# Kernel optimization log

Hardware: AMD Instinct MI355X
Metric: run time of the kernel (lower is better)

## Reference

```python
import jax, jax.numpy as jnp
import numpy as np

L, B, Q, P, D, H, F = 3, 256, 128, 16, 256, 16, 512
DK = D // H
SCALE = DK ** -0.5  # lsa=False -> constant scale
EPS = 1e-5


def _ln(x, g, b):
    m = jnp.mean(x, axis=-1, keepdims=True)
    v = jnp.mean(jnp.square(x - m), axis=-1, keepdims=True)
    return (x - m) * jax.lax.rsqrt(v + EPS) * g + b


def setup_inputs() -> dict:
    key = jax.random.key(0)
    ks = jax.random.split(key, 12)
    w = lambda k, shape: 0.02 * jax.random.normal(k, shape, dtype=jnp.float32)
    return {
        "x": jax.random.normal(ks[0], (B, Q, P), dtype=jnp.float32),
        "attn_bias": 0.1 * jax.random.normal(ks[1], (1, Q, Q), dtype=jnp.float32),
        "W_P": w(ks[2], (P, D)), "b_P": jnp.zeros((D,), jnp.float32),
        "W_pos": w(ks[3], (Q, D)),
        "Wq": w(ks[4], (L, D, D)), "bq": jnp.zeros((L, D), jnp.float32),
        "Wk": w(ks[5], (L, D, D)), "bk": jnp.zeros((L, D), jnp.float32),
        "Wv": w(ks[6], (L, D, D)), "bv": jnp.zeros((L, D), jnp.float32),
        "Wo": w(ks[7], (L, D, D)), "bo": jnp.zeros((L, D), jnp.float32),
        "ln1_g": jnp.ones((L, D), jnp.float32), "ln1_b": jnp.zeros((L, D), jnp.float32),
        "W1": w(ks[8], (L, D, F)), "b1": jnp.zeros((L, F), jnp.float32),
        "W2": w(ks[9], (L, F, D)), "b2": jnp.zeros((L, D), jnp.float32),
        "ln2_g": jnp.ones((L, D), jnp.float32), "ln2_b": jnp.zeros((L, D), jnp.float32),
    }


def _encoder(x, attn_bias, W_P, b_P, W_pos,
             Wq, bq, Wk, bk, Wv, bv, Wo, bo, ln1_g, ln1_b,
             W1, b1, W2, b2, ln2_g, ln2_b):
    # patch embedding + positional encoding (dropout=0, eval mode)
    z = x @ W_P + b_P + W_pos                      # [B, Q, D]
    bias = attn_bias[:, None]                      # [1, 1, Q, Q]

    def layer(carry, p):
        z, prev = carry
        (wq, bq_, wk, bk_, wv, bv_, wo, bo_, g1, be1, w1, b1_, w2, b2_, g2, be2) = p
        q = (z @ wq + bq_).reshape(B, Q, H, DK).transpose(0, 2, 1, 3)  # [B,H,Q,dk]
        k = (z @ wk + bk_).reshape(B, Q, H, DK).transpose(0, 2, 1, 3)
        v = (z @ wv + bv_).reshape(B, Q, H, DK).transpose(0, 2, 1, 3)
        # residual-attention + bias-augmented scores
        scores = jnp.einsum('bhqd,bhkd->bhqk', q, k) * SCALE + prev + bias
        attn = jax.nn.softmax(scores, axis=-1)
        o = jnp.einsum('bhqk,bhkd->bhqd', attn, v)
        o = o.transpose(0, 2, 1, 3).reshape(B, Q, D) @ wo + bo_
        z = _ln(z + o, g1, be1)                     # post-norm
        ffo = jax.nn.gelu(z @ w1 + b1_, approximate=False) @ w2 + b2_
        z = _ln(z + ffo, g2, be2)
        return (z, scores), None

    prev0 = jnp.zeros((B, H, Q, Q), z.dtype)        # prev=None == add zero
    params = (Wq, bq, Wk, bk, Wv, bv, Wo, bo, ln1_g, ln1_b,
              W1, b1, W2, b2, ln2_g, ln2_b)
    (z, _), _ = jax.lax.scan(layer, (z, prev0), params)
    return z


def reference(x, attn_bias, W_P, b_P, W_pos, Wq, bq, Wk, bk, Wv, bv, Wo, bo,
              ln1_g, ln1_b, W1, b1, W2, b2, ln2_g, ln2_b):
    return _encoder(x, attn_bias, W_P, b_P, W_pos, Wq, bq, Wk, bk, Wv, bv,
                    Wo, bo, ln1_g, ln1_b, W1, b1, W2, b2, ln2_g, ln2_b)
```

## Files before the change

### kernel.cpp

```cpp
#include <hip/hip_runtime.h>

#define DEV __device__ __forceinline__

typedef float          f32x4  __attribute__((ext_vector_type(4)));
typedef __bf16         bf16x8 __attribute__((ext_vector_type(8)));
typedef unsigned short u16x8  __attribute__((ext_vector_type(8)));
typedef unsigned short u16x4  __attribute__((ext_vector_type(4)));

static constexpr int  Bq   = 256;
static constexpr int  Qs   = 128;
static constexpr int  Dm   = 256;
static constexpr int  Ff   = 512;
static constexpr int  ROWS = Bq * Qs;
static constexpr long QK_LSTR = (long)ROWS * 512;

DEV float b2f(unsigned short h) {
    unsigned int u = ((unsigned int)h) << 16;
    float f; __builtin_memcpy(&f, &u, 4); return f;
}
DEV unsigned short f2b(float f) {
    unsigned int u; __builtin_memcpy(&u, &f, 4);
    u += 0x7fffu + ((u >> 16) & 1u);
    return (unsigned short)(u >> 16);
}
DEV f32x4 mfma_bf16(u16x8 a, u16x8 b, f32x4 c) {
    return __builtin_amdgcn_mfma_f32_16x16x32_bf16(
        __builtin_bit_cast(bf16x8, a), __builtin_bit_cast(bf16x8, b), c, 0, 0, 0);
}
DEV void gl_lds16(const unsigned short* g, unsigned short* l) {
    __builtin_amdgcn_global_load_lds(
        (const __attribute__((address_space(1))) unsigned int*)g,
        (__attribute__((address_space(3))) unsigned int*)l, 16, 0, 0);
}

__global__ void k_embed(const float* __restrict__ x,
                        const float* __restrict__ WP,
                        const float* __restrict__ bP,
                        const float* __restrict__ Wpos,
                        unsigned short* __restrict__ zb) {
    int row = blockIdx.x;
    int d   = threadIdx.x;
    int q   = row & (Qs - 1);
    const float* xr = x + row * 16;
    float acc = bP[d] + Wpos[q * Dm + d];
#pragma unroll
    for (int p = 0; p < 16; p++) acc += xr[p] * WP[p * Dm + d];
    zb[(long)row * Dm + d] = f2b(acc);
}

static constexpr int S0 = 3 * 768 * 256;
static constexpr int S1 = 3 * 256 * 256;
static constexpr int S2 = 3 * 512 * 256;
static constexpr int S3 = 3 * 256 * 512;
static constexpr int S4 = 3 * 768;
static constexpr int S5 = 3 * 64 * 256;
static constexpr int PREP_TOT = S0 + S1 + S2 + S3 + S4 + S5;

__global__ void k_prep(const float* __restrict__ Wq, const float* __restrict__ Wk,
                       const float* __restrict__ Wv, const float* __restrict__ Wo,
                       const float* __restrict__ W1, const float* __restrict__ W2,
                       const float* __restrict__ bq, const float* __restrict__ bk,
                       const float* __restrict__ bv, const float* __restrict__ ab,
                       unsigned short* __restrict__ wTqkv, unsigned short* __restrict__ wTo,
                       unsigned short* __restrict__ wT1, unsigned short* __restrict__ wT2,
                       float* __restrict__ bqkv, float* __restrict__ pb) {
    int idx = blockIdx.x * 256 + threadIdx.x;
    if (idx < S0) {
        int l = idx / (768 * 256), r = idx % (768 * 256);
        int n = r / 256, k = r % 256;
        const float* W = (n < 256) ? Wq : (n < 512) ? Wk : Wv;
        float v = W[(long)l * 65536 + k * 256 + (n & 255)];
        if (n < 256) v *= 0.25f;
        wTqkv[idx] = f2b(v);
    } else if (idx < S0 + S1) {
        int j = idx - S0;
        int l = j / 65536, r = j % 65536, n = r / 256, k = r % 256;
        wTo[j] = f2b(Wo[(long)l * 65536 + k * 256 + n]);
    } else if (idx < S0 + S1 + S2) {
        int j = idx - S0 - S1;
        int l = j / (512 * 256), r = j % (512 * 256), n = r / 256, k = r % 256;
        wT1[j] = f2b(W1[(long)l * 131072 + k * 512 + n]);
    } else if (idx < S0 + S1 + S2 + S3) {
        int j = idx - S0 - S1 - S2;
        int l = j / (256 * 512), r = j % (256 * 512), n = r / 512, k = r % 512;
        wT2[j] = f2b(W2[(long)l * 131072 + k * 256 + n]);
    } else if (idx < S0 + S1 + S2 + S3 + S4) {
        int j = idx - S0 - S1 - S2 - S3;
        int l = j / 768, c = j % 768;
        float v = (c < 256) ? bq[l * 256 + c] * 0.25f
                : (c < 512) ? bk[l * 256 + c - 256]
                            : bv[l * 256 + c - 512];
        bqkv[j] = v;
    } else if (idx < PREP_TOT) {
        int j = idx - S0 - S1 - S2 - S3 - S4;
        int l = j / 16384, r = j % 16384;
        int u = r / 256, t = r % 256;
        int i = u >> 5, rr = (u >> 3) & 3, jj = u & 7;
        int wave = t >> 6, quad = (t >> 4) & 3, l16 = t & 15;
        int m = 32 * wave + 16 * i + 4 * quad + rr;
        int col = 16 * jj + l16;
        pb[j] = (float)(l + 1) * ab[m * 128 + col];
    }
}

template <int GELU, int MODE>
__global__ __launch_bounds__(256) void k_gemm(const unsigned short* __restrict__ A,
                                              const unsigned short* __restrict__ WT,
                                              const float* __restrict__ bias,
                                              unsigned short* __restrict__ outB,
                                              unsigned short* __restrict__ aux,
                                              int M, int N, int K) {
    __shared__ unsigned short As[2][128 * 32];
    __shared__ unsigned short Bs[2][128 * 32];
    const int tid  = threadIdx.x;
    const int wave = tid >> 6, lane = tid & 63, quad = lane >> 4, l16 = lane & 15;
    const int mq = wave >> 1, nq = wave & 1;
    const int m_blk = blockIdx.x * 128, n_blk = blockIdx.y * 128;
    const int c0 = tid, c1 = tid + 256;
    const int ra0 = c0 >> 2, ca0 = (c0 & 3) * 8;
    const int ra1 = c1 >> 2, ca1 = (c1 & 3) * 8;

    f32x4 acc[4][4] = {};

    for (int k0 = 0; k0 < K; k0 += 64) {
#pragma unroll
        for (int hh = 0; hh < 2; hh++) {
            int kk = k0 + hh * 32;
            gl_lds16(A  + (long)(m_blk + ra0) * K + kk + ca0, &As[hh][c0 * 8]);
            gl_lds16(A  + (long)(m_blk + ra1) * K + kk + ca1, &As[hh][c1 * 8]);
            gl_lds16(WT + (long)(n_blk + ra0) * K + kk + ca0, &Bs[hh][c0 * 8]);
            gl_lds16(WT + (long)(n_blk + ra1) * K + kk + ca1, &Bs[hh][c1 * 8]);
        }
        __syncthreads();
#pragma unroll
        for (int hh = 0; hh < 2; hh++) {
            u16x8 af[4], bf[4];
#pragma unroll
            for (int i = 0; i < 4; i++)
                af[i] = *(const u16x8*)&As[hh][(64 * mq + 16 * i + l16) * 32 + quad * 8];
#pragma unroll
            for (int j = 0; j < 4; j++)
                bf[j] = *(const u16x8*)&Bs[hh][(64 * nq + 16 * j + l16) * 32 + quad * 8];
#pragma unroll
            for (int i = 0; i < 4; i++)
#pragma unroll
                for (int j = 0; j < 4; j++)
                    acc[i][j] = mfma_bf16(af[i], bf[j], acc[i][j]);
        }
        __syncthreads();
    }

#pragma unroll
    for (int i = 0; i < 4; i++) {
        int row = m_blk + 64 * mq + 16 * i + quad * 4;
#pragma unroll
        for (int j = 0; j < 4; j++) {
            int col = n_blk + 64 * nq + 16 * j + l16;
            float bb = bias[col];
#pragma unroll
            for (int r = 0; r < 4; r++) {
                float v = acc[i][j][r] + bb;
                if (GELU) v = 0.5f * v * (1.0f + erff(v * 0.70710678118f));
                if (MODE == 0) outB[(long)(row + r) * N + col] = f2b(v);
                if (MODE == 2) {
                    int grow = row + r, b = grow >> 7, rin = grow & 127;
                    if (col < 512) {
                        int s = col >> 8, hh = (col >> 4) & 15, dk = col & 15;
                        outB[((long)((b * 16 + hh) * 2 + s)) * 2048 + rin * 16 + dk] = f2b(v);
                    } else {
                        aux[(long)grow * 256 + (col - 512)] = f2b(v);
                    }
                }
            }
        }
    }
}

template <int LAST>
__global__ __launch_bounds__(256) void k_gemm_ln(const unsigned short* __restrict__ A,
                                                 const unsigned short* __restrict__ WT,
                                                 const float* __restrict__ bias,
                                                 const unsigned short* __restrict__ Zres,
                                                 const float* __restrict__ g,
                                                 const float* __restrict__ be,
                                                 unsigned short* __restrict__ zb,
                                                 float* __restrict__ outF,
                                                 int K) {
    __shared__ unsigned short smem[16384 + 2048 + 8192];
    unsigned short* Zs = smem;
    unsigned short* As = smem + 16384;
    unsigned short* Bs = smem + 16384 + 2048;
    float2* stats = (float2*)(smem + 16384);

    const int tid  = threadIdx.x;
    const int wave = tid >> 6, lane = tid & 63, quad = lane >> 4, l16 = lane & 15;
    const int m_blk = blockIdx.x * 64;

#pragma unroll
    for (int s = 0; s < 8; s++) {
        int c = tid + 256 * s;
        int zr = c >> 5, zc = (c & 31) * 8;
        gl_lds16(Zres + (long)(m_blk + zr) * 256 + zc, &Zs[c * 8]);
    }

    const int ca = (tid & 3) * 8, raA = tid >> 2;
    f32x4 acc[4][4] = {};

    for (int k0 = 0; k0 < K; k0 += 32) {
        gl_lds16(A + (long)(m_blk + raA) * K + k0 + ca, &As[tid * 8]);
#pragma unroll
        for (int s = 0; s < 4; s++) {
            int c = tid + 256 * s;
            int br = c >> 2, bc = (c & 3) * 8;
            gl_lds16(WT + (long)br * K + k0 + bc, &Bs[c * 8]);
        }
        __syncthreads();
        u16x8 af[4], bf[4];
#pragma unroll
        for (int i = 0; i < 4; i++)
            af[i] = *(const u16x8*)&As[(16 * i + l16) * 32 + quad * 8];
#pragma unroll
        for (int j = 0; j < 4; j++)
            bf[j] = *(const u16x8*)&Bs[(64 * wave + 16 * j + l16) * 32 + quad * 8];
#pragma unroll
        for (int i = 0; i < 4; i++)
#pragma unroll
            for (int j = 0; j < 4; j++)
                acc[i][j] = mfma_bf16(af[i], bf[j], acc[i][j]);
        __syncthreads();
    }

    float bb[4], gg[4], bt[4];
#pragma unroll
    for (int j = 0; j < 4; j++) {
        int col = 64 * wave + 16 * j + l16;
        bb[j] = bias[col]; gg[j] = g[col]; bt[j] = be[col];
    }
#pragma unroll
    for (int i = 0; i < 4; i++) {
#pragma unroll
        for (int r = 0; r < 4; r++) {
            int rloc = 16 * i + quad * 4 + r;
            float s1 = 0.f, s2 = 0.f;
#pragma unroll
            for (int j = 0; j < 4; j++) {
                int col = 64 * wave + 16 * j + l16;
                float v = acc[i][j][r] + bb[j] + b2f(Zs[rloc * 256 + col]);
                acc[i][j][r] = v;
                s1 += v; s2 += v * v;
            }
            for (int mk = 1; mk < 16; mk <<= 1) {
                s1 += __shfl_xor(s1, mk);
                s2 += __shfl_xor(s2, mk);
            }
            if (l16 == 0) stats[rloc * 4 + wave] = make_float2(s1, s2);
        }
    }
    __syncthreads();
#pragma unroll
    for (int i = 0; i < 4; i++) {
#pragma unroll
        for (int r = 0; r < 4; r++) {
            int rloc = 16 * i + quad * 4 + r;
            f32x4 p0 = *(const f32x4*)&stats[rloc * 4];
            f32x4 p1 = *(const f32x4*)&stats[rloc * 4 + 2];
            float S1 = p0[0] + p0[2] + p1[0] + p1[2];
            float S2 = p0[1] + p0[3] + p1[1] + p1[3];
            float mean = S1 * (1.0f / 256.0f);
            float var  = S2 * (1.0f / 256.0f) - mean * mean;
            float rstd = rsqrtf(var + 1e-5f);
            long grow = m_blk + rloc;
#pragma unroll
            for (int j = 0; j < 4; j++) {
                int col = 64 * wave + 16 * j + l16;
                float o = (acc[i][j][r] - mean) * rstd * gg[j] + bt[j];
                if (LAST) outF[grow * 256 + col] = o;
                else      zb[grow * 256 + col] = f2b(o);
            }
        }
    }
}

template <int L>
__global__ __launch_bounds__(256) void k_attn(const unsigned short* __restrict__ qkh,
                                              const unsigned short* __restrict__ vbuf,
                                              const float* __restrict__ pb,
                                              unsigned short* __restrict__ o_out) {
    __shared__ unsigned short vt[16 * 136];
    __shared__ unsigned short Ps[128 * 136];
    const int tid  = threadIdx.x;
    const int wave = tid >> 6, lane = tid & 63, quad = lane >> 4, l16 = lane & 15;
    const int b = blockIdx.x >> 4, h = blockIdx.x & 15;
    const int qrow = tid >> 1, half = tid & 1;

    u16x8 vv = *(const u16x8*)(vbuf + (long)(b * Qs + qrow) * 256 + h * 16 + half * 8);
    const float* pbt = pb + (long)L * 16384 + tid;

    f32x4 accS[2][8] = {};
    u16x8 zero = {};

    constexpr int FULL = (L + 1) / 2;
    constexpr bool HALF = ((L + 1) & 1) != 0;

#pragma unroll
    for (int p = 0; p < FULL; p++) {
        const unsigned short* q0 = qkh + ((long)(((2 * p) * Bq + b) * 16 + h) * 2) * 2048;
        const unsigned short* q1 = qkh + ((long)(((2 * p + 1) * Bq + b) * 16 + h) * 2) * 2048;
        const unsigned short* qsel = (quad < 2) ? q0 : q1;
        const unsigned short* ksel = (quad < 2) ? (q0 + 2048) : (q1 + 2048);
        const int koff = (quad & 1) * 8;
        u16x8 af[2], bf8[8];
#pragma unroll
        for (int i = 0; i < 2; i++) {
            int m = 32 * wave + 16 * i + l16;
            af[i] = *(const u16x8*)(qsel + m * 16 + koff);
        }
#pragma unroll
        for (int j = 0; j < 8; j++) {
            int n = 16 * j + l16;
            bf8[j] = *(const u16x8*)(ksel + n * 16 + koff);
        }
#pragma unroll
        for (int i = 0; i < 2; i++)
#pragma unroll
            for (int j = 0; j < 8; j++)
                accS[i][j] = mfma_bf16(af[i], bf8[j], accS[i][j]);
    }
    if (HALF) {
        const unsigned short* qt = qkh + ((long)((L * Bq + b) * 16 + h) * 2) * 2048;
        const unsigned short* kt = qt + 2048;
        u16x8 af[2], bf8[8];
#pragma unroll
        for (int i = 0; i < 2; i++) {
            int m = 32 * wave + 16 * i + l16;
            af[i] = (quad < 2) ? *(const u16x8*)(qt + m * 16 + quad * 8) : zero;
        }
#pragma unroll
        for (int j = 0; j < 8; j++) {
            int n = 16 * j + l16;
            bf8[j] = (quad < 2) ? *(const u16x8*)(kt + n * 16 + quad * 8) : zero;
        }
#pragma unroll
        for (int i = 0; i < 2; i++)
#pragma unroll
            for (int j = 0; j < 8; j++)
                accS[i][j] = mfma_bf16(af[i], bf8[j], accS[i][j]);
    }

#pragma unroll
    for (int jj = 0; jj < 8; jj++) vt[(half * 8 + jj) * 136 + qrow] = vv[jj];

#pragma unroll
    for (int i = 0; i < 2; i++) {
#pragma unroll
        for (int r = 0; r < 4; r++) {
            int m = 32 * wave + 16 * i + quad * 4 + r;
#pragma unroll
            for (int j = 0; j < 8; j++) {
                int u = (i * 4 + r) * 8 + j;
                float s = accS[i][j][r] + pbt[u * 256];
                Ps[m * 136 + 16 * j + l16] = f2b(__expf(s));
            }
        }
    }
    __syncthreads();

    f32x4 accO[2] = {};
    f32x4 accR[2] = {};
    u16x8 ones;
#pragma unroll
    for (int jj = 0; jj < 8; jj++) ones[jj] = 0x3F80;
#pragma unroll
    for (int s = 0; s < 4; s++) {
        u16x8 bv = *(const u16x8*)&vt[l16 * 136 + s * 32 + quad * 8];
#pragma unroll
        for (int i = 0; i < 2; i++) {
            u16x8 ap = *(const u16x8*)&Ps[(32 * wave + 16 * i + l16) * 136 + s * 32 + quad * 8];
            accO[i] = mfma_bf16(ap, bv, accO[i]);
            accR[i] = mfma_bf16(ap, ones, accR[i]);
        }
    }
#pragma unroll
    for (int i = 0; i < 2; i++)
#pragma unroll
        for (int r = 0; r < 4; r++) {
            int m = 32 * wave + 16 * i + quad * 4 + r;
            float inv = __builtin_amdgcn_rcpf(accR[i][r]);
            o_out[(long)(b * Qs + m) * Dm + h * 16 + l16] = f2b(accO[i][r] * inv);
        }
}

extern "C" void kernel_launch(void* const* d_in, const int* in_sizes, int n_in,
                              void* d_out, int out_size, void* d_ws, size_t ws_size,
                              hipStream_t stream) {
    const float* x     = (const float*)d_in[0];
    const float* abias = (const float*)d_in[1];
    const float* WP    = (const float*)d_in[2];
    const float* bP    = (const float*)d_in[3];
    const float* Wpos  = (const float*)d_in[4];
    const float* Wq    = (const float*)d_in[5];
    const float* bqp   = (const float*)d_in[6];
    const float* Wk    = (const float*)d_in[7];
    const float* bkp   = (const float*)d_in[8];
    const float* Wv    = (const float*)d_in[9];
    const float* bvp   = (const float*)d_in[10];
    const float* Wo    = (const float*)d_in[11];
    const float* bo    = (const float*)d_in[12];
    const float* g1    = (const float*)d_in[13];
    const float* be1   = (const float*)d_in[14];
    const float* W1    = (const float*)d_in[15];
    const float* b1    = (const float*)d_in[16];
    const float* W2    = (const float*)d_in[17];
    const float* b2    = (const float*)d_in[18];
    const float* g2    = (const float*)d_in[19];
    const float* be2   = (const float*)d_in[20];
    (void)in_sizes; (void)n_in; (void)out_size; (void)ws_size;

    char* ws = (char*)d_ws;
    size_t off = 0;
    auto alloc = [&](size_t bytes) -> char* {
        char* p = ws + off; off += (bytes + 255) & ~(size_t)255; return p;
    };
    unsigned short* z_b   = (unsigned short*)alloc((size_t)ROWS * Dm * 2);
    unsigned short* qkh   = (unsigned short*)alloc((size_t)3 * ROWS * 512 * 2);
    unsigned short* v_cur = (unsigned short*)alloc((size_t)ROWS * Dm * 2);
    unsigned short* h1    = (unsigned short*)alloc((size_t)ROWS * Ff * 2);
    unsigned short* o_b   = h1;
    unsigned short* wTqkv = (unsigned short*)alloc((size_t)S0 * 2);
    unsigned short* wTo   = (unsigned short*)alloc((size_t)S1 * 2);
    unsigned short* wT1   = (unsigned short*)alloc((size_t)S2 * 2);
    unsigned short* wT2   = (unsigned short*)alloc((size_t)S3 * 2);
    float*          bqkv  = (float*)alloc((size_t)S4 * 4);
    float*          pb    = (float*)alloc((size_t)S5 * 4);

    k_prep<<<(PREP_TOT + 255) / 256, 256, 0, stream>>>(
        Wq, Wk, Wv, Wo, W1, W2, bqp, bkp, bvp, abias,
        wTqkv, wTo, wT1, wT2, bqkv, pb);
    k_embed<<<ROWS, 256, 0, stream>>>(x, WP, bP, Wpos, z_b);

    for (int l = 0; l < 3; l++) {
        k_gemm<0, 2><<<dim3(ROWS / 128, 6), 256, 0, stream>>>(
            z_b, wTqkv + (long)l * 768 * 256, bqkv + l * 768,
            qkh + (long)l * QK_LSTR, v_cur, ROWS, 768, 256);
        if (l == 0)      k_attn<0><<<Bq * 16, 256, 0, stream>>>(qkh, v_cur, pb, o_b);
        else if (l == 1) k_attn<1><<<Bq * 16, 256, 0, stream>>>(qkh, v_cur, pb, o_b);
        else             k_attn<2><<<Bq * 16, 256, 0, stream>>>(qkh, v_cur, pb, o_b);
        k_gemm_ln<0><<<ROWS / 64, 256, 0, stream>>>(
            o_b, wTo + (long)l * 256 * 256, bo + l * 256, z_b,
            g1 + l * 256, be1 + l * 256, z_b, nullptr, 256);
        k_gemm<1, 0><<<dim3(ROWS / 128, 4), 256, 0, stream>>>(
            z_b, wT1 + (long)l * 512 * 256, b1 + l * 512, h1, nullptr, ROWS, 512, 256);
        if (l == 2)
            k_gemm_ln<1><<<ROWS / 64, 256, 0, stream>>>(
                h1, wT2 + (long)l * 256 * 512, b2 + l * 256, z_b,
                g2 + l * 256, be2 + l * 256, nullptr, (float*)d_out, 512);
        else
            k_gemm_ln<0><<<ROWS / 64, 256, 0, stream>>>(
                h1, wT2 + (long)l * 256 * 512, b2 + l * 256, z_b,
                g2 + l * 256, be2 + l * 256, z_b, nullptr, 512);
    }
}
```

Baseline: 550.6 us.

## Fuse out-proj, LN1, FFN, LN2 and next-layer QKV into one per-batch kernel

Replaces the separate GEMM and GEMM+LayerNorm launches with a single fused kernel per layer. Each 512-thread block owns one batch's 128 rows and keeps z and the FFN hidden chunk in XOR-swizzled LDS, so the FFN intermediate and z never round-trip through global memory. The same kernel also does the embedding and the next layer's QKV projection. Weights are pre-packed into MFMA-fragment order so B operands load directly from global, with no LDS staging. The trade-off is only 256 blocks with heavy LDS and register use, which lowers occupancy and drops the global-to-LDS async load pipeline.

```diff
diff --git a/kernel.cpp b/kernel.cpp
--- a/kernel.cpp
+++ b/kernel.cpp
@@ -5,7 +5,6 @@
 typedef float          f32x4  __attribute__((ext_vector_type(4)));
 typedef __bf16         bf16x8 __attribute__((ext_vector_type(8)));
 typedef unsigned short u16x8  __attribute__((ext_vector_type(8)));
-typedef unsigned short u16x4  __attribute__((ext_vector_type(4)));
 
 static constexpr int  Bq   = 256;
 static constexpr int  Qs   = 128;
@@ -27,72 +26,67 @@
     return __builtin_amdgcn_mfma_f32_16x16x32_bf16(
         __builtin_bit_cast(bf16x8, a), __builtin_bit_cast(bf16x8, b), c, 0, 0, 0);
 }
-DEV void gl_lds16(const unsigned short* g, unsigned short* l) {
-    __builtin_amdgcn_global_load_lds(
-        (const __attribute__((address_space(1))) unsigned int*)g,
-        (__attribute__((address_space(3))) unsigned int*)l, 16, 0, 0);
-}
-
-__global__ void k_embed(const float* __restrict__ x,
-                        const float* __restrict__ WP,
-                        const float* __restrict__ bP,
-                        const float* __restrict__ Wpos,
-                        unsigned short* __restrict__ zb) {
-    int row = blockIdx.x;
-    int d   = threadIdx.x;
-    int q   = row & (Qs - 1);
-    const float* xr = x + row * 16;
-    float acc = bP[d] + Wpos[q * Dm + d];
-#pragma unroll
-    for (int p = 0; p < 16; p++) acc += xr[p] * WP[p * Dm + d];
-    zb[(long)row * Dm + d] = f2b(acc);
-}
-
-static constexpr int S0 = 3 * 768 * 256;
-static constexpr int S1 = 3 * 256 * 256;
-static constexpr int S2 = 3 * 512 * 256;
-static constexpr int S3 = 3 * 256 * 512;
-static constexpr int S4 = 3 * 768;
-static constexpr int S5 = 3 * 64 * 256;
-static constexpr int PREP_TOT = S0 + S1 + S2 + S3 + S4 + S5;
+DEV int zadr(int row, int col) {
+    return row * 256 + ((((col >> 3) ^ (row & 7))) << 3) + (col & 7);
+}
+
+static constexpr int P0 = 3 * 768 * 256;
+static constexpr int P1 = 3 * 256 * 256;
+static constexpr int P2 = 3 * 512 * 256;
+static constexpr int P3 = 3 * 256 * 512;
+static constexpr int P4 = 3 * 768;
+static constexpr int P5 = 3 * 64 * 256;
+static constexpr int PREP_TOT = P0 + P1 + P2 + P3 + P4 + P5;
 
 __global__ void k_prep(const float* __restrict__ Wq, const float* __restrict__ Wk,
                        const float* __restrict__ Wv, const float* __restrict__ Wo,
                        const float* __restrict__ W1, const float* __restrict__ W2,
                        const float* __restrict__ bq, const float* __restrict__ bk,
                        const float* __restrict__ bv, const float* __restrict__ ab,
-                       unsigned short* __restrict__ wTqkv, unsigned short* __restrict__ wTo,
-                       unsigned short* __restrict__ wT1, unsigned short* __restrict__ wT2,
+                       unsigned short* __restrict__ wpQ, unsigned short* __restrict__ wpO,
+                       unsigned short* __restrict__ wp1, unsigned short* __restrict__ wp2,
                        float* __restrict__ bqkv, float* __restrict__ pb) {
     int idx = blockIdx.x * 256 + threadIdx.x;
-    if (idx < S0) {
-        int l = idx / (768 * 256), r = idx % (768 * 256);
-        int n = r / 256, k = r % 256;
-        const float* W = (n < 256) ? Wq : (n < 512) ? Wk : Wv;
-        float v = W[(long)l * 65536 + k * 256 + (n & 255)];
-        if (n < 256) v *= 0.25f;
-        wTqkv[idx] = f2b(v);
-    } else if (idx < S0 + S1) {
-        int j = idx - S0;
-        int l = j / 65536, r = j % 65536, n = r / 256, k = r % 256;
-        wTo[j] = f2b(Wo[(long)l * 65536 + k * 256 + n]);
-    } else if (idx < S0 + S1 + S2) {
-        int j = idx - S0 - S1;
-        int l = j / (512 * 256), r = j % (512 * 256), n = r / 256, k = r % 256;
-        wT1[j] = f2b(W1[(long)l * 131072 + k * 512 + n]);
-    } else if (idx < S0 + S1 + S2 + S3) {
-        int j = idx - S0 - S1 - S2;
-        int l = j / (256 * 512), r = j % (256 * 512), n = r / 512, k = r % 512;
-        wT2[j] = f2b(W2[(long)l * 131072 + k * 256 + n]);
-    } else if (idx < S0 + S1 + S2 + S3 + S4) {
-        int j = idx - S0 - S1 - S2 - S3;
+    if (idx < P0) {
+        int l = idx / 196608, r = idx % 196608;
+        int tile = r >> 9, le = r & 511, lane = le >> 3, e = le & 7;
+        int ntile = tile >> 3, kk = tile & 7;
+        int n = ntile * 16 + (lane & 15), k = kk * 32 + (lane >> 4) * 8 + e;
+        float v;
+        if (n < 256)      v = Wq[(long)l * 65536 + k * 256 + n] * 0.25f;
+        else if (n < 512) v = Wk[(long)l * 65536 + k * 256 + (n - 256)];
+        else              v = Wv[(long)l * 65536 + k * 256 + (n - 512)];
+        wpQ[idx] = f2b(v);
+    } else if (idx < P0 + P1) {
+        int j = idx - P0;
+        int l = j / 65536, r = j % 65536;
+        int tile = r >> 9, le = r & 511, lane = le >> 3, e = le & 7;
+        int ntile = tile >> 3, kk = tile & 7;
+        int n = ntile * 16 + (lane & 15), k = kk * 32 + (lane >> 4) * 8 + e;
+        wpO[j] = f2b(Wo[(long)l * 65536 + k * 256 + n]);
+    } else if (idx < P0 + P1 + P2) {
+        int j = idx - P0 - P1;
+        int l = j / 131072, r = j % 131072;
+        int tile = r >> 9, le = r & 511, lane = le >> 3, e = le & 7;
+        int ntile = tile >> 3, kk = tile & 7;
+        int n = ntile * 16 + (lane & 15), k = kk * 32 + (lane >> 4) * 8 + e;
+        wp1[j] = f2b(W1[(long)l * 131072 + k * 512 + n]);
+    } else if (idx < P0 + P1 + P2 + P3) {
+        int j = idx - P0 - P1 - P2;
+        int l = j / 131072, r = j % 131072;
+        int tile = r >> 9, le = r & 511, lane = le >> 3, e = le & 7;
+        int ntile = tile >> 4, kk = tile & 15;
+        int n = ntile * 16 + (lane & 15), k = kk * 32 + (lane >> 4) * 8 + e;
+        wp2[j] = f2b(W2[(long)l * 131072 + k * 256 + n]);
+    } else if (idx < P0 + P1 + P2 + P3 + P4) {
+        int j = idx - P0 - P1 - P2 - P3;
         int l = j / 768, c = j % 768;
         float v = (c < 256) ? bq[l * 256 + c] * 0.25f
                 : (c < 512) ? bk[l * 256 + c - 256]
                             : bv[l * 256 + c - 512];
         bqkv[j] = v;
     } else if (idx < PREP_TOT) {
-        int j = idx - S0 - S1 - S2 - S3 - S4;
+        int j = idx - P0 - P1 - P2 - P3 - P4;
         int l = j / 16384, r = j % 16384;
         int u = r / 256, t = r % 256;
         int i = u >> 5, rr = (u >> 3) & 3, jj = u & 7;
@@ -103,179 +97,273 @@
     }
 }
 
-template <int GELU, int MODE>
-__global__ __launch_bounds__(256) void k_gemm(const unsigned short* __restrict__ A,
-                                              const unsigned short* __restrict__ WT,
-                                              const float* __restrict__ bias,
-                                              unsigned short* __restrict__ outB,
-                                              unsigned short* __restrict__ aux,
-                                              int M, int N, int K) {
-    __shared__ unsigned short As[2][128 * 32];
-    __shared__ unsigned short Bs[2][128 * 32];
+template <int MODE>
+__global__ __launch_bounds__(512, 2) void k_fused(
+    const float* __restrict__ x, const float* __restrict__ WP,
+    const float* __restrict__ bP, const float* __restrict__ Wpos,
+    const unsigned short* __restrict__ zin, unsigned short* __restrict__ zout,
+    const unsigned short* __restrict__ o_b,
+    const unsigned short* __restrict__ wpO, const float* __restrict__ bo,
+    const float* __restrict__ g1, const float* __restrict__ be1,
+    const unsigned short* __restrict__ wp1, const float* __restrict__ b1,
+    const unsigned short* __restrict__ wp2, const float* __restrict__ b2,
+    const float* __restrict__ g2, const float* __restrict__ be2,
+    const unsigned short* __restrict__ wpQ, const float* __restrict__ bq,
+    unsigned short* __restrict__ qkh, unsigned short* __restrict__ vcur,
+    float* __restrict__ outf) {
+    __shared__ unsigned short zs[128 * 256];
+    __shared__ unsigned short hcs[128 * 256];
+    float2* stats = (float2*)hcs;
+
     const int tid  = threadIdx.x;
-    const int wave = tid >> 6, lane = tid & 63, quad = lane >> 4, l16 = lane & 15;
-    const int mq = wave >> 1, nq = wave & 1;
-    const int m_blk = blockIdx.x * 128, n_blk = blockIdx.y * 128;
-    const int c0 = tid, c1 = tid + 256;
-    const int ra0 = c0 >> 2, ca0 = (c0 & 3) * 8;
-    const int ra1 = c1 >> 2, ca1 = (c1 & 3) * 8;
-
-    f32x4 acc[4][4] = {};
-
-    for (int k0 = 0; k0 < K; k0 += 64) {
-#pragma unroll
-        for (int hh = 0; hh < 2; hh++) {
-            int kk = k0 + hh * 32;
-            gl_lds16(A  + (long)(m_blk + ra0) * K + kk + ca0, &As[hh][c0 * 8]);
-            gl_lds16(A  + (long)(m_blk + ra1) * K + kk + ca1, &As[hh][c1 * 8]);
-            gl_lds16(WT + (long)(n_blk + ra0) * K + kk + ca0, &Bs[hh][c0 * 8]);
-            gl_lds16(WT + (long)(n_blk + ra1) * K + kk + ca1, &Bs[hh][c1 * 8]);
+    const int wave = tid >> 6, lane = tid & 63, quad = (tid >> 4) & 3, l16 = tid & 15;
+    const int b = blockIdx.x;
+    const long rbase = (long)b * 128;
+
+    if constexpr (MODE == 0) {
+        int row = tid >> 2;
+        const float* xr = x + (rbase + row) * 16;
+        float xl[16];
+#pragma unroll
+        for (int p = 0; p < 16; p++) xl[p] = xr[p];
+#pragma unroll
+        for (int cc = 0; cc < 8; cc++) {
+            int c0 = (tid & 3) * 64 + cc * 8;
+            u16x8 pk;
+#pragma unroll
+            for (int e = 0; e < 8; e++) {
+                int c = c0 + e;
+                float a = bP[c] + Wpos[row * 256 + c];
+#pragma unroll
+                for (int p = 0; p < 16; p++) a += xl[p] * WP[p * 256 + c];
+                pk[e] = f2b(a);
+            }
+            *(u16x8*)&zs[zadr(row, c0)] = pk;
+            *(u16x8*)&zout[(rbase + row) * 256 + c0] = pk;
         }
         __syncthreads();
-#pragma unroll
-        for (int hh = 0; hh < 2; hh++) {
-            u16x8 af[4], bf[4];
-#pragma unroll
-            for (int i = 0; i < 4; i++)
-                af[i] = *(const u16x8*)&As[hh][(64 * mq + 16 * i + l16) * 32 + quad * 8];
-#pragma unroll
-            for (int j = 0; j < 4; j++)
-                bf[j] = *(const u16x8*)&Bs[hh][(64 * nq + 16 * j + l16) * 32 + quad * 8];
-#pragma unroll
-            for (int i = 0; i < 4; i++)
-#pragma unroll
-                for (int j = 0; j < 4; j++)
-                    acc[i][j] = mfma_bf16(af[i], bf[j], acc[i][j]);
+    } else {
+        int row = tid >> 2;
+#pragma unroll
+        for (int cc = 0; cc < 8; cc++) {
+            int c0 = (tid & 3) * 64 + cc * 8;
+            u16x8 v = *(const u16x8*)&zin[(rbase + row) * 256 + c0];
+            *(u16x8*)&zs[zadr(row, c0)] = v;
         }
         __syncthreads();
     }
 
-#pragma unroll
-    for (int i = 0; i < 4; i++) {
-        int row = m_blk + 64 * mq + 16 * i + quad * 4;
-#pragma unroll
-        for (int j = 0; j < 4; j++) {
-            int col = n_blk + 64 * nq + 16 * j + l16;
-            float bb = bias[col];
+    if constexpr (MODE >= 1) {
+        f32x4 acc[8][2] = {};
+        {
+            const unsigned short* ob = o_b + rbase * 256;
+#pragma unroll 2
+            for (int kk = 0; kk < 8; kk++) {
+                u16x8 af[8], bf[2];
+#pragma unroll
+                for (int i = 0; i < 8; i++)
+                    af[i] = *(const u16x8*)&ob[(16 * i + l16) * 256 + kk * 32 + quad * 8];
+#pragma unroll
+                for (int j = 0; j < 2; j++)
+                    bf[j] = *(const u16x8*)&wpO[((2 * wave + j) * 8 + kk) * 512 + lane * 8];
+#pragma unroll
+                for (int i = 0; i < 8; i++)
+#pragma unroll
+                    for (int j = 0; j < 2; j++)
+                        acc[i][j] = mfma_bf16(af[i], bf[j], acc[i][j]);
+            }
+        }
+        float bo2[2], gg[2], bb[2];
+#pragma unroll
+        for (int j = 0; j < 2; j++) {
+            int col = 32 * wave + 16 * j + l16;
+            bo2[j] = bo[col]; gg[j] = g1[col]; bb[j] = be1[col];
+        }
+#pragma unroll
+        for (int i = 0; i < 8; i++)
 #pragma unroll
             for (int r = 0; r < 4; r++) {
-                float v = acc[i][j][r] + bb;
-                if (GELU) v = 0.5f * v * (1.0f + erff(v * 0.70710678118f));
-                if (MODE == 0) outB[(long)(row + r) * N + col] = f2b(v);
-                if (MODE == 2) {
-                    int grow = row + r, b = grow >> 7, rin = grow & 127;
-                    if (col < 512) {
-                        int s = col >> 8, hh = (col >> 4) & 15, dk = col & 15;
-                        outB[((long)((b * 16 + hh) * 2 + s)) * 2048 + rin * 16 + dk] = f2b(v);
+                int row = 16 * i + quad * 4 + r;
+                float s1 = 0.f, s2 = 0.f;
+#pragma unroll
+                for (int j = 0; j < 2; j++) {
+                    int col = 32 * wave + 16 * j + l16;
+                    float v = acc[i][j][r] + bo2[j] + b2f(zs[zadr(row, col)]);
+                    acc[i][j][r] = v; s1 += v; s2 += v * v;
+                }
+                for (int mk = 1; mk < 16; mk <<= 1) { s1 += __shfl_xor(s1, mk); s2 += __shfl_xor(s2, mk); }
+                if (l16 == 0) stats[row * 8 + wave] = make_float2(s1, s2);
+            }
+        __syncthreads();
+#pragma unroll
+        for (int i = 0; i < 8; i++)
+#pragma unroll
+            for (int r = 0; r < 4; r++) {
+                int row = 16 * i + quad * 4 + r;
+                f32x4 p0 = *(const f32x4*)&stats[row * 8];
+                f32x4 p1 = *(const f32x4*)&stats[row * 8 + 2];
+                f32x4 p2 = *(const f32x4*)&stats[row * 8 + 4];
+                f32x4 p3 = *(const f32x4*)&stats[row * 8 + 6];
+                float S1 = p0[0] + p0[2] + p1[0] + p1[2] + p2[0] + p2[2] + p3[0] + p3[2];
+                float S2 = p0[1] + p0[3] + p1[1] + p1[3] + p2[1] + p2[3] + p3[1] + p3[3];
+                float mean = S1 * (1.0f / 256.0f);
+                float var  = S2 * (1.0f / 256.0f) - mean * mean;
+                float rstd = rsqrtf(var + 1e-5f);
+#pragma unroll
+                for (int j = 0; j < 2; j++) {
+                    int col = 32 * wave + 16 * j + l16;
+                    zs[zadr(row, col)] = f2b((acc[i][j][r] - mean) * rstd * gg[j] + bb[j]);
+                }
+            }
+        __syncthreads();
+
+        f32x4 z2[8][2] = {};
+#pragma unroll
+        for (int c = 0; c < 2; c++) {
+            f32x4 a1[8][2] = {};
+#pragma unroll 2
+            for (int kk = 0; kk < 8; kk++) {
+                u16x8 af[8], bf[2];
+#pragma unroll
+                for (int i = 0; i < 8; i++)
+                    af[i] = *(const u16x8*)&zs[(16 * i + l16) * 256 + (((kk * 4 + quad) ^ (l16 & 7)) << 3)];
+#pragma unroll
+                for (int j = 0; j < 2; j++)
+                    bf[j] = *(const u16x8*)&wp1[((16 * c + 2 * wave + j) * 8 + kk) * 512 + lane * 8];
+#pragma unroll
+                for (int i = 0; i < 8; i++)
+#pragma unroll
+                    for (int j = 0; j < 2; j++)
+                        a1[i][j] = mfma_bf16(af[i], bf[j], a1[i][j]);
+            }
+            float b1v[2];
+#pragma unroll
+            for (int j = 0; j < 2; j++) b1v[j] = b1[256 * c + 32 * wave + 16 * j + l16];
+#pragma unroll
+            for (int i = 0; i < 8; i++)
+#pragma unroll
+                for (int j = 0; j < 2; j++)
+#pragma unroll
+                    for (int r = 0; r < 4; r++) {
+                        int row = 16 * i + quad * 4 + r;
+                        int colh = 32 * wave + 16 * j + l16;
+                        float v = a1[i][j][r] + b1v[j];
+                        float gel = 0.5f * v * (1.0f + erff(v * 0.70710678118f));
+                        hcs[zadr(row, colh)] = f2b(gel);
+                    }
+            __syncthreads();
+#pragma unroll 2
+            for (int kk = 0; kk < 8; kk++) {
+                u16x8 af[8], bf[2];
+#pragma unroll
+                for (int i = 0; i < 8; i++)
+                    af[i] = *(const u16x8*)&hcs[(16 * i + l16) * 256 + (((kk * 4 + quad) ^ (l16 & 7)) << 3)];
+#pragma unroll
+                for (int j = 0; j < 2; j++)
+                    bf[j] = *(const u16x8*)&wp2[((2 * wave + j) * 16 + 8 * c + kk) * 512 + lane * 8];
+#pragma unroll
+                for (int i = 0; i < 8; i++)
+#pragma unroll
+                    for (int j = 0; j < 2; j++)
+                        z2[i][j] = mfma_bf16(af[i], bf[j], z2[i][j]);
+            }
+            __syncthreads();
+        }
+
+        float b2v[2], gg2[2], bb2[2];
+#pragma unroll
+        for (int j = 0; j < 2; j++) {
+            int col = 32 * wave + 16 * j + l16;
+            b2v[j] = b2[col]; gg2[j] = g2[col]; bb2[j] = be2[col];
+        }
+#pragma unroll
+        for (int i = 0; i < 8; i++)
+#pragma unroll
+            for (int r = 0; r < 4; r++) {
+                int row = 16 * i + quad * 4 + r;
+                float s1 = 0.f, s2 = 0.f;
+#pragma unroll
+                for (int j = 0; j < 2; j++) {
+                    int col = 32 * wave + 16 * j + l16;
+                    float v = z2[i][j][r] + b2v[j] + b2f(zs[zadr(row, col)]);
+                    z2[i][j][r] = v; s1 += v; s2 += v * v;
+                }
+                for (int mk = 1; mk < 16; mk <<= 1) { s1 += __shfl_xor(s1, mk); s2 += __shfl_xor(s2, mk); }
+                if (l16 == 0) stats[row * 8 + wave] = make_float2(s1, s2);
+            }
+        __syncthreads();
+#pragma unroll
+        for (int i = 0; i < 8; i++)
+#pragma unroll
+            for (int r = 0; r < 4; r++) {
+                int row = 16 * i + quad * 4 + r;
+                f32x4 p0 = *(const f32x4*)&stats[row * 8];
+                f32x4 p1 = *(const f32x4*)&stats[row * 8 + 2];
+                f32x4 p2 = *(const f32x4*)&stats[row * 8 + 4];
+                f32x4 p3 = *(const f32x4*)&stats[row * 8 + 6];
+                float S1 = p0[0] + p0[2] + p1[0] + p1[2] + p2[0] + p2[2] + p3[0] + p3[2];
+                float S2 = p0[1] + p0[3] + p1[1] + p1[3] + p2[1] + p2[3] + p3[1] + p3[3];
+                float mean = S1 * (1.0f / 256.0f);
+                float var  = S2 * (1.0f / 256.0f) - mean * mean;
+                float rstd = rsqrtf(var + 1e-5f);
+#pragma unroll
+                for (int j = 0; j < 2; j++) {
+                    int col = 32 * wave + 16 * j + l16;
+                    float o = (z2[i][j][r] - mean) * rstd * gg2[j] + bb2[j];
+                    if constexpr (MODE == 2) {
+                        outf[(rbase + row) * 256 + col] = o;
                     } else {
-                        aux[(long)grow * 256 + (col - 512)] = f2b(v);
+                        unsigned short hv = f2b(o);
+                        zs[zadr(row, col)] = hv;
+                        zout[(rbase + row) * 256 + col] = hv;
                     }
                 }
             }
-        }
-    }
-}
-
-template <int LAST>
-__global__ __launch_bounds__(256) void k_gemm_ln(const unsigned short* __restrict__ A,
-                                                 const unsigned short* __restrict__ WT,
-                                                 const float* __restrict__ bias,
-                                                 const unsigned short* __restrict__ Zres,
-                                                 const float* __restrict__ g,
-                                                 const float* __restrict__ be,
-                                                 unsigned short* __restrict__ zb,
-                                                 float* __restrict__ outF,
-                                                 int K) {
-    __shared__ unsigned short smem[16384 + 2048 + 8192];
-    unsigned short* Zs = smem;
-    unsigned short* As = smem + 16384;
-    unsigned short* Bs = smem + 16384 + 2048;
-    float2* stats = (float2*)(smem + 16384);
-
-    const int tid  = threadIdx.x;
-    const int wave = tid >> 6, lane = tid & 63, quad = lane >> 4, l16 = lane & 15;
-    const int m_blk = blockIdx.x * 64;
-
-#pragma unroll
-    for (int s = 0; s < 8; s++) {
-        int c = tid + 256 * s;
-        int zr = c >> 5, zc = (c & 31) * 8;
-        gl_lds16(Zres + (long)(m_blk + zr) * 256 + zc, &Zs[c * 8]);
-    }
-
-    const int ca = (tid & 3) * 8, raA = tid >> 2;
-    f32x4 acc[4][4] = {};
-
-    for (int k0 = 0; k0 < K; k0 += 32) {
-        gl_lds16(A + (long)(m_blk + raA) * K + k0 + ca, &As[tid * 8]);
-#pragma unroll
-        for (int s = 0; s < 4; s++) {
-            int c = tid + 256 * s;
-            int br = c >> 2, bc = (c & 3) * 8;
-            gl_lds16(WT + (long)br * K + k0 + bc, &Bs[c * 8]);
-        }
-        __syncthreads();
-        u16x8 af[4], bf[4];
-#pragma unroll
-        for (int i = 0; i < 4; i++)
-            af[i] = *(const u16x8*)&As[(16 * i + l16) * 32 + quad * 8];
-#pragma unroll
-        for (int j = 0; j < 4; j++)
-            bf[j] = *(const u16x8*)&Bs[(64 * wave + 16 * j + l16) * 32 + quad * 8];
-#pragma unroll
-        for (int i = 0; i < 4; i++)
-#pragma unroll
-            for (int j = 0; j < 4; j++)
-                acc[i][j] = mfma_bf16(af[i], bf[j], acc[i][j]);
-        __syncthreads();
-    }
-
-    float bb[4], gg[4], bt[4];
-#pragma unroll
-    for (int j = 0; j < 4; j++) {
-        int col = 64 * wave + 16 * j + l16;
-        bb[j] = bias[col]; gg[j] = g[col]; bt[j] = be[col];
-    }
-#pragma unroll
-    for (int i = 0; i < 4; i++) {
-#pragma unroll
-        for (int r = 0; r < 4; r++) {
-            int rloc = 16 * i + quad * 4 + r;
-            float s1 = 0.f, s2 = 0.f;
-#pragma unroll
-            for (int j = 0; j < 4; j++) {
-                int col = 64 * wave + 16 * j + l16;
-                float v = acc[i][j][r] + bb[j] + b2f(Zs[rloc * 256 + col]);
-                acc[i][j][r] = v;
-                s1 += v; s2 += v * v;
-            }
-            for (int mk = 1; mk < 16; mk <<= 1) {
-                s1 += __shfl_xor(s1, mk);
-                s2 += __shfl_xor(s2, mk);
-            }
-            if (l16 == 0) stats[rloc * 4 + wave] = make_float2(s1, s2);
-        }
-    }
-    __syncthreads();
-#pragma unroll
-    for (int i = 0; i < 4; i++) {
-#pragma unroll
-        for (int r = 0; r < 4; r++) {
-            int rloc = 16 * i + quad * 4 + r;
-            f32x4 p0 = *(const f32x4*)&stats[rloc * 4];
-            f32x4 p1 = *(const f32x4*)&stats[rloc * 4 + 2];
-            float S1 = p0[0] + p0[2] + p1[0] + p1[2];
-            float S2 = p0[1] + p0[3] + p1[1] + p1[3];
-            float mean = S1 * (1.0f / 256.0f);
-            float var  = S2 * (1.0f / 256.0f) - mean * mean;
-            float rstd = rsqrtf(var + 1e-5f);
-            long grow = m_blk + rloc;
-#pragma unroll
-            for (int j = 0; j < 4; j++) {
-                int col = 64 * wave + 16 * j + l16;
-                float o = (acc[i][j][r] - mean) * rstd * gg[j] + bt[j];
-                if (LAST) outF[grow * 256 + col] = o;
-                else      zb[grow * 256 + col] = f2b(o);
+        if constexpr (MODE == 1) __syncthreads();
+    }
+
+    if constexpr (MODE <= 1) {
+#pragma unroll
+        for (int p = 0; p < 2; p++) {
+            f32x4 aq[8][3] = {};
+#pragma unroll 2
+            for (int kk = 0; kk < 8; kk++) {
+                u16x8 af[8], bf[3];
+#pragma unroll
+                for (int i = 0; i < 8; i++)
+                    af[i] = *(const u16x8*)&zs[(16 * i + l16) * 256 + (((kk * 4 + quad) ^ (l16 & 7)) << 3)];
+#pragma unroll
+                for (int j = 0; j < 3; j++)
+                    bf[j] = *(const u16x8*)&wpQ[((6 * wave + 3 * p + j) * 8 + kk) * 512 + lane * 8];
+#pragma unroll
+                for (int i = 0; i < 8; i++)
+#pragma unroll
+                    for (int j = 0; j < 3; j++)
+                        aq[i][j] = mfma_bf16(af[i], bf[j], aq[i][j]);
+            }
+#pragma unroll
+            for (int j = 0; j < 3; j++) {
+                int col = 96 * wave + 48 * p + 16 * j + l16;
+                float bqv = bq[col];
+                if (col < 512) {
+                    int s = col >> 8, hh = (col >> 4) & 15, dk = col & 15;
+                    unsigned short* qk = qkh + ((long)((b * 16 + hh) * 2 + s)) * 2048;
+#pragma unroll
+                    for (int i = 0; i < 8; i++)
+#pragma unroll
+                        for (int r = 0; r < 4; r++) {
+                            int rin = 16 * i + quad * 4 + r;
+                            qk[rin * 16 + dk] = f2b(aq[i][j][r] + bqv);
+                        }
+                } else {
+#pragma unroll
+                    for (int i = 0; i < 8; i++)
+#pragma unroll
+                        for (int r = 0; r < 4; r++) {
+                            int rin = 16 * i + quad * 4 + r;
+                            vcur[(rbase + rin) * 256 + (col - 512)] = f2b(aq[i][j][r] + bqv);
+                        }
+                }
             }
         }
     }
@@ -424,39 +512,47 @@
     unsigned short* z_b   = (unsigned short*)alloc((size_t)ROWS * Dm * 2);
     unsigned short* qkh   = (unsigned short*)alloc((size_t)3 * ROWS * 512 * 2);
     unsigned short* v_cur = (unsigned short*)alloc((size_t)ROWS * Dm * 2);
-    unsigned short* h1    = (unsigned short*)alloc((size_t)ROWS * Ff * 2);
-    unsigned short* o_b   = h1;
-    unsigned short* wTqkv = (unsigned short*)alloc((size_t)S0 * 2);
-    unsigned short* wTo   = (unsigned short*)alloc((size_t)S1 * 2);
-    unsigned short* wT1   = (unsigned short*)alloc((size_t)S2 * 2);
-    unsigned short* wT2   = (unsigned short*)alloc((size_t)S3 * 2);
-    float*          bqkv  = (float*)alloc((size_t)S4 * 4);
-    float*          pb    = (float*)alloc((size_t)S5 * 4);
+    unsigned short* o_b   = (unsigned short*)alloc((size_t)ROWS * Dm * 2);
+    unsigned short* wpQ   = (unsigned short*)alloc((size_t)P0 * 2);
+    unsigned short* wpO   = (unsigned short*)alloc((size_t)P1 * 2);
+    unsigned short* wp1   = (unsigned short*)alloc((size_t)P2 * 2);
+    unsigned short* wp2   = (unsigned short*)alloc((size_t)P3 * 2);
+    float*          bqkv  = (float*)alloc((size_t)P4 * 4);
+    float*          pb    = (float*)alloc((size_t)P5 * 4);
 
     k_prep<<<(PREP_TOT + 255) / 256, 256, 0, stream>>>(
         Wq, Wk, Wv, Wo, W1, W2, bqp, bkp, bvp, abias,
-        wTqkv, wTo, wT1, wT2, bqkv, pb);
-    k_embed<<<ROWS, 256, 0, stream>>>(x, WP, bP, Wpos, z_b);
+        wpQ, wpO, wp1, wp2, bqkv, pb);
+
+    k_fused<0><<<256, 512, 0, stream>>>(
+        x, WP, bP, Wpos,
+        nullptr, z_b, nullptr,
+        nullptr, nullptr, nullptr, nullptr,
+        nullptr, nullptr, nullptr, nullptr, nullptr, nullptr,
+        wpQ, bqkv, qkh, v_cur, nullptr);
 
     for (int l = 0; l < 3; l++) {
-        k_gemm<0, 2><<<dim3(ROWS / 128, 6), 256, 0, stream>>>(
-            z_b, wTqkv + (long)l * 768 * 256, bqkv + l * 768,
-            qkh + (long)l * QK_LSTR, v_cur, ROWS, 768, 256);
         if (l == 0)      k_attn<0><<<Bq * 16, 256, 0, stream>>>(qkh, v_cur, pb, o_b);
         else if (l == 1) k_attn<1><<<Bq * 16, 256, 0, stream>>>(qkh, v_cur, pb, o_b);
         else             k_attn<2><<<Bq * 16, 256, 0, stream>>>(qkh, v_cur, pb, o_b);
-        k_gemm_ln<0><<<ROWS / 64, 256, 0, stream>>>(
-            o_b, wTo + (long)l * 256 * 256, bo + l * 256, z_b,
-            g1 + l * 256, be1 + l * 256, z_b, nullptr, 256);
-        k_gemm<1, 0><<<dim3(ROWS / 128, 4), 256, 0, stream>>>(
-            z_b, wT1 + (long)l * 512 * 256, b1 + l * 512, h1, nullptr, ROWS, 512, 256);
-        if (l == 2)
-            k_gemm_ln<1><<<ROWS / 64, 256, 0, stream>>>(
-                h1, wT2 + (long)l * 256 * 512, b2 + l * 256, z_b,
-                g2 + l * 256, be2 + l * 256, nullptr, (float*)d_out, 512);
-        else
-            k_gemm_ln<0><<<ROWS / 64, 256, 0, stream>>>(
-                h1, wT2 + (long)l * 256 * 512, b2 + l * 256, z_b,
-                g2 + l * 256, be2 + l * 256, z_b, nullptr, 512);
-    }
-}
+
+        if (l < 2) {
+            k_fused<1><<<256, 512, 0, stream>>>(
+                nullptr, nullptr, nullptr, nullptr,
+                z_b, z_b, o_b,
+                wpO + (long)l * 65536, bo + l * 256, g1 + l * 256, be1 + l * 256,
+                wp1 + (long)l * 131072, b1 + l * 512,
+                wp2 + (long)l * 131072, b2 + l * 256, g2 + l * 256, be2 + l * 256,
+                wpQ + (long)(l + 1) * 196608, bqkv + (l + 1) * 768,
+                qkh + (long)(l + 1) * QK_LSTR, v_cur, nullptr);
+        } else {
+            k_fused<2><<<256, 512, 0, stream>>>(
+                nullptr, nullptr, nullptr, nullptr,
+                z_b, nullptr, o_b,
+                wpO + (long)l * 65536, bo + l * 256, g1 + l * 256, be1 + l * 256,
+                wp1 + (long)l * 131072, b1 + l * 512,
+                wp2 + (long)l * 131072, b2 + l * 256, g2 + l * 256, be2 + l * 256,
+                nullptr, nullptr, nullptr, nullptr, (float*)d_out);
+        }
+    }
+}
```

Result: slower. 804.6 us (+46.1%).

## Stage GEMM and attention epilogues through LDS for coalesced head-major stores

Applied to the files above, without the earlier changes.

GEMM epilogues now write results into shared memory and then emit 16-byte vectorized global stores, replacing scattered 2-byte stores. V and the attention output switch to a head-major layout ([head][row][16]), so attention can read V and write O contiguously per block. The output-projection GEMM+LN kernel gains a template path that reads A in this head-major layout. This aims to cut uncoalesced memory traffic in the epilogues, at the cost of extra LDS round trips and barriers.

```diff
diff --git a/kernel.cpp b/kernel.cpp
--- a/kernel.cpp
+++ b/kernel.cpp
@@ -5,7 +5,6 @@
 typedef float          f32x4  __attribute__((ext_vector_type(4)));
 typedef __bf16         bf16x8 __attribute__((ext_vector_type(8)));
 typedef unsigned short u16x8  __attribute__((ext_vector_type(8)));
-typedef unsigned short u16x4  __attribute__((ext_vector_type(4)));
 
 static constexpr int  Bq   = 256;
 static constexpr int  Qs   = 128;
@@ -110,8 +109,9 @@
                                               unsigned short* __restrict__ outB,
                                               unsigned short* __restrict__ aux,
                                               int M, int N, int K) {
-    __shared__ unsigned short As[2][128 * 32];
-    __shared__ unsigned short Bs[2][128 * 32];
+    __shared__ unsigned short smem[16384];
+    unsigned short* As = smem;
+    unsigned short* Bs = smem + 8192;
     const int tid  = threadIdx.x;
     const int wave = tid >> 6, lane = tid & 63, quad = lane >> 4, l16 = lane & 15;
     const int mq = wave >> 1, nq = wave & 1;
@@ -126,10 +126,10 @@
 #pragma unroll
         for (int hh = 0; hh < 2; hh++) {
             int kk = k0 + hh * 32;
-            gl_lds16(A  + (long)(m_blk + ra0) * K + kk + ca0, &As[hh][c0 * 8]);
-            gl_lds16(A  + (long)(m_blk + ra1) * K + kk + ca1, &As[hh][c1 * 8]);
-            gl_lds16(WT + (long)(n_blk + ra0) * K + kk + ca0, &Bs[hh][c0 * 8]);
-            gl_lds16(WT + (long)(n_blk + ra1) * K + kk + ca1, &Bs[hh][c1 * 8]);
+            gl_lds16(A  + (long)(m_blk + ra0) * K + kk + ca0, &As[hh * 4096 + c0 * 8]);
+            gl_lds16(A  + (long)(m_blk + ra1) * K + kk + ca1, &As[hh * 4096 + c1 * 8]);
+            gl_lds16(WT + (long)(n_blk + ra0) * K + kk + ca0, &Bs[hh * 4096 + c0 * 8]);
+            gl_lds16(WT + (long)(n_blk + ra1) * K + kk + ca1, &Bs[hh * 4096 + c1 * 8]);
         }
         __syncthreads();
 #pragma unroll
@@ -137,10 +137,10 @@
             u16x8 af[4], bf[4];
 #pragma unroll
             for (int i = 0; i < 4; i++)
-                af[i] = *(const u16x8*)&As[hh][(64 * mq + 16 * i + l16) * 32 + quad * 8];
+                af[i] = *(const u16x8*)&As[hh * 4096 + (64 * mq + 16 * i + l16) * 32 + quad * 8];
 #pragma unroll
             for (int j = 0; j < 4; j++)
-                bf[j] = *(const u16x8*)&Bs[hh][(64 * nq + 16 * j + l16) * 32 + quad * 8];
+                bf[j] = *(const u16x8*)&Bs[hh * 4096 + (64 * nq + 16 * j + l16) * 32 + quad * 8];
 #pragma unroll
             for (int i = 0; i < 4; i++)
 #pragma unroll
@@ -152,31 +152,46 @@
 
 #pragma unroll
     for (int i = 0; i < 4; i++) {
-        int row = m_blk + 64 * mq + 16 * i + quad * 4;
+        int rl = 64 * mq + 16 * i + quad * 4;
 #pragma unroll
         for (int j = 0; j < 4; j++) {
-            int col = n_blk + 64 * nq + 16 * j + l16;
-            float bb = bias[col];
+            int cl = 64 * nq + 16 * j + l16;
+            float bb = bias[n_blk + cl];
 #pragma unroll
             for (int r = 0; r < 4; r++) {
                 float v = acc[i][j][r] + bb;
                 if (GELU) v = 0.5f * v * (1.0f + erff(v * 0.70710678118f));
-                if (MODE == 0) outB[(long)(row + r) * N + col] = f2b(v);
+                if (MODE == 0) smem[(rl + r) * 128 + cl] = f2b(v);
                 if (MODE == 2) {
-                    int grow = row + r, b = grow >> 7, rin = grow & 127;
-                    if (col < 512) {
-                        int s = col >> 8, hh = (col >> 4) & 15, dk = col & 15;
-                        outB[((long)((b * 16 + hh) * 2 + s)) * 2048 + rin * 16 + dk] = f2b(v);
-                    } else {
-                        aux[(long)grow * 256 + (col - 512)] = f2b(v);
-                    }
+                    int g = 4 * nq + j;
+                    smem[g * 2048 + (rl + r) * 16 + l16] = f2b(v);
                 }
             }
         }
     }
-}
-
-template <int LAST>
+    __syncthreads();
+#pragma unroll
+    for (int c = tid; c < 2048; c += 256) {
+        u16x8 val = *(const u16x8*)&smem[c * 8];
+        if (MODE == 0) {
+            int row = c >> 4, seg = c & 15;
+            *(u16x8*)&outB[(long)(m_blk + row) * N + n_blk + seg * 8] = val;
+        }
+        if (MODE == 2) {
+            int g = c >> 8, w = c & 255;
+            int n = n_blk + g * 16;
+            if (n < 512) {
+                int s = n >> 8, h = (n >> 4) & 15;
+                *(u16x8*)&outB[((long)(((m_blk >> 7) * 16 + h) * 2 + s)) * 2048 + w * 8] = val;
+            } else {
+                int hh = (n - 512) >> 4;
+                *(u16x8*)&aux[((long)hh * ROWS + m_blk) * 16 + w * 8] = val;
+            }
+        }
+    }
+}
+
+template <int LAST, int AHM>
 __global__ __launch_bounds__(256) void k_gemm_ln(const unsigned short* __restrict__ A,
                                                  const unsigned short* __restrict__ WT,
                                                  const float* __restrict__ bias,
@@ -207,7 +222,12 @@
     f32x4 acc[4][4] = {};
 
     for (int k0 = 0; k0 < K; k0 += 32) {
-        gl_lds16(A + (long)(m_blk + raA) * K + k0 + ca, &As[tid * 8]);
+        if (AHM) {
+            int k = k0 + ca;
+            gl_lds16(A + ((long)(k >> 4) * ROWS + m_blk + raA) * 16 + (k & 15), &As[tid * 8]);
+        } else {
+            gl_lds16(A + (long)(m_blk + raA) * K + k0 + ca, &As[tid * 8]);
+        }
 #pragma unroll
         for (int s = 0; s < 4; s++) {
             int c = tid + 256 * s;
@@ -293,7 +313,7 @@
     const int b = blockIdx.x >> 4, h = blockIdx.x & 15;
     const int qrow = tid >> 1, half = tid & 1;
 
-    u16x8 vv = *(const u16x8*)(vbuf + (long)(b * Qs + qrow) * 256 + h * 16 + half * 8);
+    u16x8 vv = *(const u16x8*)(vbuf + ((long)h * ROWS + b * Qs + qrow) * 16 + half * 8);
     const float* pbt = pb + (long)L * 16384 + tid;
 
     f32x4 accS[2][8] = {};
@@ -380,14 +400,20 @@
             accR[i] = mfma_bf16(ap, ones, accR[i]);
         }
     }
+    __syncthreads();
 #pragma unroll
     for (int i = 0; i < 2; i++)
 #pragma unroll
         for (int r = 0; r < 4; r++) {
             int m = 32 * wave + 16 * i + quad * 4 + r;
             float inv = __builtin_amdgcn_rcpf(accR[i][r]);
-            o_out[(long)(b * Qs + m) * Dm + h * 16 + l16] = f2b(accO[i][r] * inv);
-        }
+            vt[m * 16 + l16] = f2b(accO[i][r] * inv);
+        }
+    __syncthreads();
+    {
+        unsigned short* obase = o_out + ((long)h * ROWS + b * Qs) * 16;
+        *(u16x8*)&obase[tid * 8] = *(const u16x8*)&vt[tid * 8];
+    }
 }
 
 extern "C" void kernel_launch(void* const* d_in, const int* in_sizes, int n_in,
@@ -445,17 +471,17 @@
         if (l == 0)      k_attn<0><<<Bq * 16, 256, 0, stream>>>(qkh, v_cur, pb, o_b);
         else if (l == 1) k_attn<1><<<Bq * 16, 256, 0, stream>>>(qkh, v_cur, pb, o_b);
         else             k_attn<2><<<Bq * 16, 256, 0, stream>>>(qkh, v_cur, pb, o_b);
-        k_gemm_ln<0><<<ROWS / 64, 256, 0, stream>>>(
+        k_gemm_ln<0, 1><<<ROWS / 64, 256, 0, stream>>>(
             o_b, wTo + (long)l * 256 * 256, bo + l * 256, z_b,
             g1 + l * 256, be1 + l * 256, z_b, nullptr, 256);
         k_gemm<1, 0><<<dim3(ROWS / 128, 4), 256, 0, stream>>>(
             z_b, wT1 + (long)l * 512 * 256, b1 + l * 512, h1, nullptr, ROWS, 512, 256);
         if (l == 2)
-            k_gemm_ln<1><<<ROWS / 64, 256, 0, stream>>>(
+            k_gemm_ln<1, 0><<<ROWS / 64, 256, 0, stream>>>(
                 h1, wT2 + (long)l * 256 * 512, b2 + l * 256, z_b,
                 g2 + l * 256, be2 + l * 256, nullptr, (float*)d_out, 512);
         else
-            k_gemm_ln<0><<<ROWS / 64, 256, 0, stream>>>(
+            k_gemm_ln<0, 0><<<ROWS / 64, 256, 0, stream>>>(
                 h1, wT2 + (long)l * 256 * 512, b2 + l * 256, z_b,
                 g2 + l * 256, be2 + l * 256, z_b, nullptr, 512);
     }
```

Measured after the change: 550.5 us. No clear change (-0.0%).
